# Optimization experiments

Measured on AMD Instinct MI355X. Metric: run time of the kernel, lower is better.

Reference implementation:

```python
import jax, jax.numpy as jnp
import numpy as np

N_HEADS = 16
DIM = 1024
NEG_INF = -1e20  # neginf for fp32 per original module


def setup_inputs() -> dict:
    key = jax.random.key(0)
    ks = jax.random.split(key, 10)
    B, N, D = 2, 2048, DIM
    std = np.sqrt(2.0 / (D + D))  # xavier_normal for square weights
    inp = {
        "query": jax.random.normal(ks[0], (B, N, D), dtype=jnp.float32),
        "mask": jax.random.randint(ks[1], (B, N), 0, 2, dtype=jnp.int32),
        "wq": jax.random.normal(ks[2], (D, D), dtype=jnp.float32) * std,
        "bq": jnp.zeros((D,), dtype=jnp.float32),
        "wk": jax.random.normal(ks[3], (D, D), dtype=jnp.float32) * std,
        "bk": jnp.zeros((D,), dtype=jnp.float32),
        "wv": jax.random.normal(ks[4], (D, D), dtype=jnp.float32) * std,
        "bv": jnp.zeros((D,), dtype=jnp.float32),
        "wo": jax.random.normal(ks[5], (D, D), dtype=jnp.float32) * std,
        "bo": jnp.zeros((D,), dtype=jnp.float32),
    }
    return inp


def reference(query, mask, wq, bq, wk, bk, wv, bv, wo, bo):
    B, N, D = query.shape
    H = N_HEADS
    dh = D // H
    scale = jnp.asarray(np.sqrt(dh), dtype=query.dtype)

    def heads(x):  # [B,N,D] -> [B,H,N,dh]
        return x.reshape(B, N, H, dh).transpose(0, 2, 1, 3)

    q = heads(query @ wq.T + bq) / scale
    k = heads(query @ wk.T + bk)
    v = heads(query @ wv.T + bv)

    # [B,H,Nq,Nk] scaled dot-product scores, masked where mask==0
    dot_prod = jnp.einsum("bhqd,bhkd->bhqk", q, k)
    dot_prod = jnp.where(mask[:, None, None, :] == 0, NEG_INF, dot_prod)

    attn = jax.nn.softmax(dot_prod.astype(jnp.float32), axis=-1).astype(query.dtype)
    # dropout p=0 -> identity
    ctx = jnp.einsum("bhqk,bhkd->bhqd", attn, v)
    ctx = ctx.transpose(0, 2, 1, 3).reshape(B, N, D)
    out = ctx @ wo.T + bo
    # original returns dot_prod as [B*H, Nq, Nk]
    return out, dot_prod.reshape(B * H, N, N)
```

## Files before the change

### kernel.cpp

```cpp
#include <hip/hip_runtime.h>

typedef unsigned short u16;
typedef unsigned int u32;
typedef __attribute__((ext_vector_type(8))) __bf16 bf16x8;
typedef __attribute__((ext_vector_type(4))) float f32x4;

#define MFMA(a, b, c) __builtin_amdgcn_mfma_f32_16x16x32_bf16((a), (b), (c), 0, 0, 0)

__device__ __forceinline__ u16 f2bf(float f) {
  union { float f; unsigned u; } v; v.f = f;
  unsigned r = v.u + 0x7fffu + ((v.u >> 16) & 1u);
  return (u16)(r >> 16);
}

__device__ __forceinline__ void gld16(const u16* g, u16* l) {
  __builtin_amdgcn_global_load_lds(
      (const __attribute__((address_space(1))) unsigned int*)(g),
      (__attribute__((address_space(3))) unsigned int*)(l), 16, 0, 0);
}

__global__ __launch_bounds__(256) void k_cast(
    const float* __restrict__ query, const float* __restrict__ wq,
    const float* __restrict__ wk, const float* __restrict__ wv,
    const float* __restrict__ wo, u16* __restrict__ dst)
{
  size_t i = ((size_t)blockIdx.x * 256 + threadIdx.x) * 8;
  const float* src; size_t off; float sc = 1.0f;
  if (i < 4194304u)      { src = query; off = i; }
  else if (i < 5242880u) { src = wq; off = i - 4194304u; sc = 0.125f; }
  else if (i < 6291456u) { src = wk; off = i - 5242880u; }
  else if (i < 7340032u) { src = wv; off = i - 6291456u; }
  else                   { src = wo; off = i - 7340032u; }
  float4 a = *(const float4*)(src + off);
  float4 b = *(const float4*)(src + off + 4);
  alignas(16) u16 r[8] = { f2bf(a.x*sc), f2bf(a.y*sc), f2bf(a.z*sc), f2bf(a.w*sc),
                           f2bf(b.x*sc), f2bf(b.y*sc), f2bf(b.z*sc), f2bf(b.w*sc) };
  *(int4*)(dst + i) = *(int4*)r;
}

__global__ __launch_bounds__(256) void k_gemm_qkv(
    const u16* __restrict__ Ab, const u16* __restrict__ Wb,
    const float* __restrict__ bq, const float* __restrict__ bk, const float* __restrict__ bv,
    u16* __restrict__ Qh, u16* __restrict__ Kh, u16* __restrict__ Vt)
{
  const int fb = blockIdx.x;
  const int sb = (fb & 7) * 96 + (fb >> 3);
  const int n0 = (sb % 24) * 128;
  const int m0 = (sb / 24) * 128;
  const int tid = threadIdx.x;
  const int w = tid >> 6, lane = tid & 63, g = lane >> 4, l15 = lane & 15;
  const int wm = w >> 1, wn = w & 1;
  __shared__ alignas(16) u16 As[128 * 32];
  __shared__ alignas(16) u16 Bs[128 * 32];
  f32x4 acc[4][4] = {};
  for (int k0 = 0; k0 < 1024; k0 += 32) {
    __syncthreads();
#pragma unroll
    for (int t = 0; t < 2; ++t) {
      int i = t * 256 + tid;
      int row = i >> 2, ch = i & 3, sch = ch ^ (row & 3);
      gld16(Ab + (size_t)(m0 + row) * 1024 + k0 + sch * 8, As + i * 8);
    }
#pragma unroll
    for (int t = 0; t < 2; ++t) {
      int i = t * 256 + tid;
      int row = i >> 2, ch = i & 3, sch = ch ^ (row & 3);
      gld16(Wb + (size_t)(n0 + row) * 1024 + k0 + sch * 8, Bs + i * 8);
    }
    __syncthreads();
    bf16x8 af[4], bfr[4];
#pragma unroll
    for (int i = 0; i < 4; ++i) {
      int row = wm * 64 + i * 16 + l15;
      af[i] = *(const bf16x8*)(As + (row * 4 + (g ^ (row & 3))) * 8);
    }
#pragma unroll
    for (int j = 0; j < 4; ++j) {
      int row = wn * 64 + j * 16 + l15;
      bfr[j] = *(const bf16x8*)(Bs + (row * 4 + (g ^ (row & 3))) * 8);
    }
#pragma unroll
    for (int i = 0; i < 4; ++i)
#pragma unroll
      for (int j = 0; j < 4; ++j)
        acc[i][j] = MFMA(af[i], bfr[j], acc[i][j]);
  }
  const int proj = n0 >> 10;
  const float* bias = (proj == 0) ? bq : (proj == 1) ? bk : bv;
  const float bsc = (proj == 0) ? 0.125f : 1.0f;
#pragma unroll
  for (int i = 0; i < 4; ++i)
#pragma unroll
    for (int j = 0; j < 4; ++j)
#pragma unroll
      for (int jj = 0; jj < 4; ++jj) {
        int mr = m0 + wm * 64 + i * 16 + g * 4 + jj;
        int c  = n0 + wn * 64 + j * 16 + l15;
        int d = c & 1023, h = d >> 6, d64 = d & 63;
        int b = mr >> 11, n = mr & 2047;
        int bh = (b << 4) | h;
        float v = acc[i][j][jj] + bias[d] * bsc;
        if (proj == 2) {
          Vt[((size_t)bh * 64 + d64) * 2048 + n] = f2bf(v);
        } else {
          u16* dst = (proj == 0) ? Qh : Kh;
          dst[((size_t)bh * 2048 + n) * 64 + d64] = f2bf(v);
        }
      }
}

__global__ __launch_bounds__(256) void k_gemm_out(
    const u16* __restrict__ Ab, const u16* __restrict__ Wb,
    const float* __restrict__ bo, float* __restrict__ out)
{
  const int fb = blockIdx.x;
  const int sb = (fb & 7) * 32 + (fb >> 3);
  const int n0 = (sb & 7) * 128;
  const int m0 = (sb >> 3) * 128;
  const int tid = threadIdx.x;
  const int w = tid >> 6, lane = tid & 63, g = lane >> 4, l15 = lane & 15;
  const int wm = w >> 1, wn = w & 1;
  __shared__ alignas(16) u16 As[128 * 32];
  __shared__ alignas(16) u16 Bs[128 * 32];
  f32x4 acc[4][4] = {};
  for (int k0 = 0; k0 < 1024; k0 += 32) {
    __syncthreads();
#pragma unroll
    for (int t = 0; t < 2; ++t) {
      int i = t * 256 + tid;
      int row = i >> 2, ch = i & 3, sch = ch ^ (row & 3);
      gld16(Ab + (size_t)(m0 + row) * 1024 + k0 + sch * 8, As + i * 8);
    }
#pragma unroll
    for (int t = 0; t < 2; ++t) {
      int i = t * 256 + tid;
      int row = i >> 2, ch = i & 3, sch = ch ^ (row & 3);
      gld16(Wb + (size_t)(n0 + row) * 1024 + k0 + sch * 8, Bs + i * 8);
    }
    __syncthreads();
    bf16x8 af[4], bfr[4];
#pragma unroll
    for (int i = 0; i < 4; ++i) {
      int row = wm * 64 + i * 16 + l15;
      af[i] = *(const bf16x8*)(As + (row * 4 + (g ^ (row & 3))) * 8);
    }
#pragma unroll
    for (int j = 0; j < 4; ++j) {
      int row = wn * 64 + j * 16 + l15;
      bfr[j] = *(const bf16x8*)(Bs + (row * 4 + (g ^ (row & 3))) * 8);
    }
#pragma unroll
    for (int i = 0; i < 4; ++i)
#pragma unroll
      for (int j = 0; j < 4; ++j)
        acc[i][j] = MFMA(af[i], bfr[j], acc[i][j]);
  }
#pragma unroll
  for (int i = 0; i < 4; ++i)
#pragma unroll
    for (int j = 0; j < 4; ++j)
#pragma unroll
      for (int jj = 0; jj < 4; ++jj) {
        int mr = m0 + wm * 64 + i * 16 + g * 4 + jj;
        int c  = n0 + wn * 64 + j * 16 + l15;
        out[(size_t)mr * 1024 + c] = acc[i][j][jj] + bo[c];
      }
}

__global__ __launch_bounds__(256) void k_attn(
    const u16* __restrict__ Qh, const u16* __restrict__ Kh, const u16* __restrict__ Vt,
    const int* __restrict__ mask, float* __restrict__ dout, u16* __restrict__ ctx)
{
  const int fb = blockIdx.x;
  const int sb = (fb & 7) * 128 + (fb >> 3);
  const int qt = sb & 31;
  const int bh = sb >> 5;
  const int b  = bh >> 4;
  const int tid = threadIdx.x;
  const int w = tid >> 6, lane = tid & 63, g = lane >> 4, l15 = lane & 15;
  __shared__ alignas(16) u16 Ks[128 * 64];
  __shared__ alignas(16) u16 Vs[64 * 128];
  __shared__ alignas(16) u16 Ps[4][16 * 140];

  const u16* Qrow = Qh + ((size_t)bh * 2048 + qt * 64 + w * 16 + l15) * 64;
  bf16x8 qf0 = *(const bf16x8*)(Qrow + g * 8);
  bf16x8 qf1 = *(const bf16x8*)(Qrow + 32 + g * 8);

  float m[4] = {-3e38f, -3e38f, -3e38f, -3e38f};
  float l[4] = {0.f, 0.f, 0.f, 0.f};
  f32x4 O[4] = {};
  const int* maskb = mask + b * 2048;
  float* Sbase = dout + 4194304 + (size_t)bh * 4194304
               + (size_t)(qt * 64 + w * 16 + g * 4) * 2048 + l15;

  for (int kt = 0; kt < 16; ++kt) {
    __syncthreads();
    const u16* Kg = Kh + ((size_t)bh * 2048 + kt * 128) * 64;
#pragma unroll
    for (int it = 0; it < 4; ++it) {
      int i = it * 256 + tid;
      int row = i >> 3, ch = i & 7, sch = ch ^ (row & 7);
      gld16(Kg + row * 64 + sch * 8, Ks + i * 8);
    }
    const u16* Vg = Vt + (size_t)bh * 131072 + kt * 128;
#pragma unroll
    for (int it = 0; it < 4; ++it) {
      int i = it * 256 + tid;
      int row = i >> 4, ch = i & 15, sch = ch ^ (row & 15);
      gld16(Vg + (size_t)row * 2048 + sch * 8, Vs + i * 8);
    }
    int mk[8];
#pragma unroll
    for (int f = 0; f < 8; ++f) mk[f] = maskb[kt * 128 + f * 16 + l15];
    __syncthreads();

    f32x4 s[8];
#pragma unroll
    for (int f = 0; f < 8; ++f) {
      int row = f * 16 + l15;
      bf16x8 kf0 = *(const bf16x8*)(Ks + (row * 8 + ((0 + g) ^ (row & 7))) * 8);
      bf16x8 kf1 = *(const bf16x8*)(Ks + (row * 8 + ((4 + g) ^ (row & 7))) * 8);
      f32x4 t = {};
      t = MFMA(qf0, kf0, t);
      t = MFMA(qf1, kf1, t);
      s[f] = t;
    }

    float fb8[8];
#pragma unroll
    for (int f = 0; f < 8; ++f) fb8[f] = (mk[f] != 0) ? 0.f : -1e20f;

    float mloc[4] = {-3e38f, -3e38f, -3e38f, -3e38f};
#pragma unroll
    for (int jj = 0; jj < 4; ++jj)
#pragma unroll
      for (int f = 0; f < 8; ++f) {
        float sv = s[f][jj] + fb8[f];
        s[f][jj] = sv;
        __builtin_nontemporal_store(sv, &Sbase[(size_t)jj * 2048 + kt * 128 + f * 16]);
        mloc[jj] = fmaxf(mloc[jj], sv);
      }
#pragma unroll
    for (int d = 1; d < 16; d <<= 1)
#pragma unroll
      for (int jj = 0; jj < 4; ++jj)
        mloc[jj] = fmaxf(mloc[jj], __shfl_xor(mloc[jj], d, 64));

    float corr[4];
#pragma unroll
    for (int jj = 0; jj < 4; ++jj) {
      float mn = fmaxf(m[jj], mloc[jj]);
      corr[jj] = __expf(m[jj] - mn);
      m[jj] = mn;
    }
    float psum[4] = {0.f, 0.f, 0.f, 0.f};
#pragma unroll
    for (int f = 0; f < 8; ++f)
#pragma unroll
      for (int jj = 0; jj < 4; ++jj) {
        float p = __expf(s[f][jj] - m[jj]);
        psum[jj] += p;
        Ps[w][(g * 4 + jj) * 140 + f * 16 + l15] = f2bf(p);
      }
#pragma unroll
    for (int d = 1; d < 16; d <<= 1)
#pragma unroll
      for (int jj = 0; jj < 4; ++jj)
        psum[jj] += __shfl_xor(psum[jj], d, 64);
#pragma unroll
    for (int jj = 0; jj < 4; ++jj) l[jj] = l[jj] * corr[jj] + psum[jj];
#pragma unroll
    for (int fd = 0; fd < 4; ++fd)
#pragma unroll
      for (int jj = 0; jj < 4; ++jj) O[fd][jj] *= corr[jj];

#pragma unroll
    for (int fk = 0; fk < 4; ++fk) {
      bf16x8 pa = *(const bf16x8*)(&Ps[w][l15 * 140 + fk * 32 + g * 8]);
#pragma unroll
      for (int fd = 0; fd < 4; ++fd) {
        int row = fd * 16 + l15;
        bf16x8 bv = *(const bf16x8*)(Vs + (row * 16 + ((fk * 4 + g) ^ (row & 15))) * 8);
        O[fd] = MFMA(pa, bv, O[fd]);
      }
    }
  }
  float inv[4];
#pragma unroll
  for (int jj = 0; jj < 4; ++jj) inv[jj] = 1.0f / l[jj];
  const int h = bh & 15;
#pragma unroll
  for (int fd = 0; fd < 4; ++fd)
#pragma unroll
    for (int jj = 0; jj < 4; ++jj) {
      int n = qt * 64 + w * 16 + g * 4 + jj;
      int c = h * 64 + fd * 16 + l15;
      ctx[((size_t)(b * 2048 + n)) * 1024 + c] = f2bf(O[fd][jj] * inv[jj]);
    }
}

extern "C" void kernel_launch(void* const* d_in, const int* in_sizes, int n_in,
                              void* d_out, int out_size, void* d_ws, size_t ws_size,
                              hipStream_t stream)
{
  const float* query = (const float*)d_in[0];
  const int*   mask  = (const int*)d_in[1];
  const float* wq = (const float*)d_in[2];
  const float* bq = (const float*)d_in[3];
  const float* wk = (const float*)d_in[4];
  const float* bk = (const float*)d_in[5];
  const float* wv = (const float*)d_in[6];
  const float* bv = (const float*)d_in[7];
  const float* wo = (const float*)d_in[8];
  const float* bo = (const float*)d_in[9];
  float* out = (float*)d_out;

  u16* ws   = (u16*)d_ws;
  u16* Ab   = ws;
  u16* Wqkv = ws + 4194304;
  u16* Wo   = ws + 7340032;
  u16* Qh   = ws + 8388608;
  u16* Kh   = ws + 12582912;
  u16* Vt   = ws + 16777216;
  u16* ctx  = ws + 20971520;

  k_cast<<<4096, 256, 0, stream>>>(query, wq, wk, wv, wo, ws);
  k_gemm_qkv<<<768, 256, 0, stream>>>(Ab, Wqkv, bq, bk, bv, Qh, Kh, Vt);
  k_attn<<<1024, 256, 0, stream>>>(Qh, Kh, Vt, mask, out, ctx);
  k_gemm_out<<<256, 256, 0, stream>>>(ctx, Wo, bo, out);
}
```

Baseline: 210.2 us.

## Process two 64-row query groups per attention block to reuse K/V tiles

```diff
diff --git a/kernel.cpp b/kernel.cpp
--- a/kernel.cpp
+++ b/kernel.cpp
@@ -172,9 +172,9 @@
     const int* __restrict__ mask, float* __restrict__ dout, u16* __restrict__ ctx)
 {
   const int fb = blockIdx.x;
-  const int sb = (fb & 7) * 128 + (fb >> 3);
-  const int qt = sb & 31;
-  const int bh = sb >> 5;
+  const int sb = (fb & 7) * 64 + (fb >> 3);
+  const int qt = sb & 15;
+  const int bh = sb >> 4;
   const int b  = bh >> 4;
   const int tid = threadIdx.x;
   const int w = tid >> 6, lane = tid & 63, g = lane >> 4, l15 = lane & 15;
@@ -182,16 +182,24 @@
   __shared__ alignas(16) u16 Vs[64 * 128];
   __shared__ alignas(16) u16 Ps[4][16 * 140];
 
-  const u16* Qrow = Qh + ((size_t)bh * 2048 + qt * 64 + w * 16 + l15) * 64;
-  bf16x8 qf0 = *(const bf16x8*)(Qrow + g * 8);
-  bf16x8 qf1 = *(const bf16x8*)(Qrow + 32 + g * 8);
-
-  float m[4] = {-3e38f, -3e38f, -3e38f, -3e38f};
-  float l[4] = {0.f, 0.f, 0.f, 0.f};
-  f32x4 O[4] = {};
+  bf16x8 qf0[2], qf1[2];
+#pragma unroll
+  for (int grp = 0; grp < 2; ++grp) {
+    const u16* Qrow = Qh + ((size_t)bh * 2048 + qt * 128 + grp * 64 + w * 16 + l15) * 64;
+    qf0[grp] = *(const bf16x8*)(Qrow + g * 8);
+    qf1[grp] = *(const bf16x8*)(Qrow + 32 + g * 8);
+  }
+
+  float m[2][4], l[2][4];
+  f32x4 O[2][4] = {};
+#pragma unroll
+  for (int grp = 0; grp < 2; ++grp)
+#pragma unroll
+    for (int jj = 0; jj < 4; ++jj) { m[grp][jj] = -3e38f; l[grp][jj] = 0.f; }
+
   const int* maskb = mask + b * 2048;
-  float* Sbase = dout + 4194304 + (size_t)bh * 4194304
-               + (size_t)(qt * 64 + w * 16 + g * 4) * 2048 + l15;
+  float* Sb0 = dout + 4194304 + (size_t)bh * 4194304
+             + (size_t)(qt * 128 + w * 16 + g * 4) * 2048 + l15;
 
   for (int kt = 0; kt < 16; ++kt) {
     __syncthreads();
@@ -212,91 +220,97 @@
     int mk[8];
 #pragma unroll
     for (int f = 0; f < 8; ++f) mk[f] = maskb[kt * 128 + f * 16 + l15];
-    __syncthreads();
-
-    f32x4 s[8];
-#pragma unroll
-    for (int f = 0; f < 8; ++f) {
-      int row = f * 16 + l15;
-      bf16x8 kf0 = *(const bf16x8*)(Ks + (row * 8 + ((0 + g) ^ (row & 7))) * 8);
-      bf16x8 kf1 = *(const bf16x8*)(Ks + (row * 8 + ((4 + g) ^ (row & 7))) * 8);
-      f32x4 t = {};
-      t = MFMA(qf0, kf0, t);
-      t = MFMA(qf1, kf1, t);
-      s[f] = t;
-    }
-
     float fb8[8];
 #pragma unroll
     for (int f = 0; f < 8; ++f) fb8[f] = (mk[f] != 0) ? 0.f : -1e20f;
-
-    float mloc[4] = {-3e38f, -3e38f, -3e38f, -3e38f};
-#pragma unroll
-    for (int jj = 0; jj < 4; ++jj)
+    __syncthreads();
+
+#pragma unroll
+    for (int grp = 0; grp < 2; ++grp) {
+      f32x4 s[8];
 #pragma unroll
       for (int f = 0; f < 8; ++f) {
-        float sv = s[f][jj] + fb8[f];
-        s[f][jj] = sv;
-        __builtin_nontemporal_store(sv, &Sbase[(size_t)jj * 2048 + kt * 128 + f * 16]);
-        mloc[jj] = fmaxf(mloc[jj], sv);
-      }
-#pragma unroll
-    for (int d = 1; d < 16; d <<= 1)
+        int row = f * 16 + l15;
+        bf16x8 kf0 = *(const bf16x8*)(Ks + (row * 8 + ((0 + g) ^ (row & 7))) * 8);
+        bf16x8 kf1 = *(const bf16x8*)(Ks + (row * 8 + ((4 + g) ^ (row & 7))) * 8);
+        f32x4 t = {};
+        t = MFMA(qf0[grp], kf0, t);
+        t = MFMA(qf1[grp], kf1, t);
+        s[f] = t;
+      }
+
+      float* Sbase = Sb0 + (size_t)grp * 64 * 2048;
+      float mloc[4] = {-3e38f, -3e38f, -3e38f, -3e38f};
 #pragma unroll
       for (int jj = 0; jj < 4; ++jj)
-        mloc[jj] = fmaxf(mloc[jj], __shfl_xor(mloc[jj], d, 64));
-
-    float corr[4];
-#pragma unroll
-    for (int jj = 0; jj < 4; ++jj) {
-      float mn = fmaxf(m[jj], mloc[jj]);
-      corr[jj] = __expf(m[jj] - mn);
-      m[jj] = mn;
-    }
-    float psum[4] = {0.f, 0.f, 0.f, 0.f};
-#pragma unroll
-    for (int f = 0; f < 8; ++f)
+#pragma unroll
+        for (int f = 0; f < 8; ++f) {
+          float sv = s[f][jj] + fb8[f];
+          s[f][jj] = sv;
+          __builtin_nontemporal_store(sv, &Sbase[(size_t)jj * 2048 + kt * 128 + f * 16]);
+          mloc[jj] = fmaxf(mloc[jj], sv);
+        }
+#pragma unroll
+      for (int d = 1; d < 16; d <<= 1)
+#pragma unroll
+        for (int jj = 0; jj < 4; ++jj)
+          mloc[jj] = fmaxf(mloc[jj], __shfl_xor(mloc[jj], d, 64));
+
+      float corr[4];
 #pragma unroll
       for (int jj = 0; jj < 4; ++jj) {
-        float p = __expf(s[f][jj] - m[jj]);
-        psum[jj] += p;
-        Ps[w][(g * 4 + jj) * 140 + f * 16 + l15] = f2bf(p);
-      }
-#pragma unroll
-    for (int d = 1; d < 16; d <<= 1)
-#pragma unroll
-      for (int jj = 0; jj < 4; ++jj)
-        psum[jj] += __shfl_xor(psum[jj], d, 64);
-#pragma unroll
-    for (int jj = 0; jj < 4; ++jj) l[jj] = l[jj] * corr[jj] + psum[jj];
+        float mn = fmaxf(m[grp][jj], mloc[jj]);
+        corr[jj] = __expf(m[grp][jj] - mn);
+        m[grp][jj] = mn;
+      }
+      float psum[4] = {0.f, 0.f, 0.f, 0.f};
+#pragma unroll
+      for (int f = 0; f < 8; ++f)
+#pragma unroll
+        for (int jj = 0; jj < 4; ++jj) {
+          float p = __expf(s[f][jj] - m[grp][jj]);
+          psum[jj] += p;
+          Ps[w][(g * 4 + jj) * 140 + f * 16 + l15] = f2bf(p);
+        }
+#pragma unroll
+      for (int d = 1; d < 16; d <<= 1)
+#pragma unroll
+        for (int jj = 0; jj < 4; ++jj)
+          psum[jj] += __shfl_xor(psum[jj], d, 64);
+#pragma unroll
+      for (int jj = 0; jj < 4; ++jj) l[grp][jj] = l[grp][jj] * corr[jj] + psum[jj];
+#pragma unroll
+      for (int fd = 0; fd < 4; ++fd)
+#pragma unroll
+        for (int jj = 0; jj < 4; ++jj) O[grp][fd][jj] *= corr[jj];
+
+#pragma unroll
+      for (int fk = 0; fk < 4; ++fk) {
+        bf16x8 pa = *(const bf16x8*)(&Ps[w][l15 * 140 + fk * 32 + g * 8]);
+#pragma unroll
+        for (int fd = 0; fd < 4; ++fd) {
+          int row = fd * 16 + l15;
+          bf16x8 bv = *(const bf16x8*)(Vs + (row * 16 + ((fk * 4 + g) ^ (row & 15))) * 8);
+          O[grp][fd] = MFMA(pa, bv, O[grp][fd]);
+        }
+      }
+    }
+  }
+  const int h = bh & 15;
+#pragma unroll
+  for (int grp = 0; grp < 2; ++grp) {
+    float inv[4];
+#pragma unroll
+    for (int jj = 0; jj < 4; ++jj) inv[jj] = 1.0f / l[grp][jj];
 #pragma unroll
     for (int fd = 0; fd < 4; ++fd)
 #pragma unroll
-      for (int jj = 0; jj < 4; ++jj) O[fd][jj] *= corr[jj];
-
-#pragma unroll
-    for (int fk = 0; fk < 4; ++fk) {
-      bf16x8 pa = *(const bf16x8*)(&Ps[w][l15 * 140 + fk * 32 + g * 8]);
-#pragma unroll
-      for (int fd = 0; fd < 4; ++fd) {
-        int row = fd * 16 + l15;
-        bf16x8 bv = *(const bf16x8*)(Vs + (row * 16 + ((fk * 4 + g) ^ (row & 15))) * 8);
-        O[fd] = MFMA(pa, bv, O[fd]);
-      }
-    }
-  }
-  float inv[4];
-#pragma unroll
-  for (int jj = 0; jj < 4; ++jj) inv[jj] = 1.0f / l[jj];
-  const int h = bh & 15;
-#pragma unroll
-  for (int fd = 0; fd < 4; ++fd)
-#pragma unroll
-    for (int jj = 0; jj < 4; ++jj) {
-      int n = qt * 64 + w * 16 + g * 4 + jj;
-      int c = h * 64 + fd * 16 + l15;
-      ctx[((size_t)(b * 2048 + n)) * 1024 + c] = f2bf(O[fd][jj] * inv[jj]);
-    }
+      for (int jj = 0; jj < 4; ++jj) {
+        int n = qt * 128 + grp * 64 + w * 16 + g * 4 + jj;
+        int c = h * 64 + fd * 16 + l15;
+        ctx[((size_t)(b * 2048 + n)) * 1024 + c] = f2bf(O[grp][fd][jj] * inv[jj]);
+      }
+  }
 }
 
 extern "C" void kernel_launch(void* const* d_in, const int* in_sizes, int n_in,
@@ -326,6 +340,6 @@
 
   k_cast<<<4096, 256, 0, stream>>>(query, wq, wk, wv, wo, ws);
   k_gemm_qkv<<<768, 256, 0, stream>>>(Ab, Wqkv, bq, bk, bv, Qh, Kh, Vt);
-  k_attn<<<1024, 256, 0, stream>>>(Qh, Kh, Vt, mask, out, ctx);
+  k_attn<<<512, 256, 0, stream>>>(Qh, Kh, Vt, mask, out, ctx);
   k_gemm_out<<<256, 256, 0, stream>>>(ctx, Wo, bo, out);
 }
```

Measured after the change: 211.7 us. No clear change (+0.7%).

## Double-buffer QKV GEMM with 256x256 tiles and interleaved prefetch

Applied to the files above, without the earlier changes.

```diff
diff --git a/kernel.cpp b/kernel.cpp
--- a/kernel.cpp
+++ b/kernel.cpp
@@ -38,68 +38,136 @@
   *(int4*)(dst + i) = *(int4*)r;
 }
 
-__global__ __launch_bounds__(256) void k_gemm_qkv(
+__global__ __launch_bounds__(512, 2) void k_gemm_qkv(
     const u16* __restrict__ Ab, const u16* __restrict__ Wb,
     const float* __restrict__ bq, const float* __restrict__ bk, const float* __restrict__ bv,
     u16* __restrict__ Qh, u16* __restrict__ Kh, u16* __restrict__ Vt)
 {
   const int fb = blockIdx.x;
-  const int sb = (fb & 7) * 96 + (fb >> 3);
-  const int n0 = (sb % 24) * 128;
-  const int m0 = (sb / 24) * 128;
+  const int sb = (fb & 7) * 24 + (fb >> 3);
+  const int n0 = (sb % 12) * 256;
+  const int m0 = (sb / 12) * 256;
   const int tid = threadIdx.x;
-  const int w = tid >> 6, lane = tid & 63, g = lane >> 4, l15 = lane & 15;
-  const int wm = w >> 1, wn = w & 1;
-  __shared__ alignas(16) u16 As[128 * 32];
-  __shared__ alignas(16) u16 Bs[128 * 32];
-  f32x4 acc[4][4] = {};
-  for (int k0 = 0; k0 < 1024; k0 += 32) {
-    __syncthreads();
+  const int wid = tid >> 6, lane = tid & 63, g = lane >> 4, l15 = lane & 15;
+  const int wm = wid >> 2, wn = wid & 3;
+  __shared__ alignas(16) u16 As[2][256 * 64];
+  __shared__ alignas(16) u16 Bs[2][256 * 64];
+
+  auto stageA = [&](int buf, int half, int k0) {
 #pragma unroll
     for (int t = 0; t < 2; ++t) {
-      int i = t * 256 + tid;
-      int row = i >> 2, ch = i & 3, sch = ch ^ (row & 3);
-      gld16(Ab + (size_t)(m0 + row) * 1024 + k0 + sch * 8, As + i * 8);
-    }
+      int i = t * 512 + tid;
+      int row = i >> 3, ch = i & 7;
+      gld16(Ab + (size_t)(m0 + half * 128 + row) * 1024 + k0 + ((ch ^ (row & 7)) * 8),
+            &As[buf][(half * 128 + row) * 64 + ch * 8]);
+    }
+  };
+  auto stageB = [&](int buf, int half, int k0) {
 #pragma unroll
     for (int t = 0; t < 2; ++t) {
-      int i = t * 256 + tid;
-      int row = i >> 2, ch = i & 3, sch = ch ^ (row & 3);
-      gld16(Wb + (size_t)(n0 + row) * 1024 + k0 + sch * 8, Bs + i * 8);
-    }
-    __syncthreads();
-    bf16x8 af[4], bfr[4];
-#pragma unroll
-    for (int i = 0; i < 4; ++i) {
-      int row = wm * 64 + i * 16 + l15;
-      af[i] = *(const bf16x8*)(As + (row * 4 + (g ^ (row & 3))) * 8);
-    }
-#pragma unroll
-    for (int j = 0; j < 4; ++j) {
-      int row = wn * 64 + j * 16 + l15;
-      bfr[j] = *(const bf16x8*)(Bs + (row * 4 + (g ^ (row & 3))) * 8);
-    }
-#pragma unroll
-    for (int i = 0; i < 4; ++i)
-#pragma unroll
-      for (int j = 0; j < 4; ++j)
-        acc[i][j] = MFMA(af[i], bfr[j], acc[i][j]);
+      int i = t * 512 + tid;
+      int row = i >> 3, ch = i & 7;
+      gld16(Wb + (size_t)(n0 + half * 128 + row) * 1024 + k0 + ((ch ^ (row & 7)) * 8),
+            &Bs[buf][(half * 128 + row) * 64 + ch * 8]);
+    }
+  };
+
+  f32x4 acc[8][4] = {};
+  stageA(0, 0, 0); stageA(0, 1, 0); stageB(0, 0, 0); stageB(0, 1, 0);
+  __syncthreads();
+
+  int cur = 0;
+  for (int ks = 0; ks < 16; ++ks) {
+    const int nxt = cur ^ 1;
+    const bool pf = (ks < 15);
+    const int kn = (ks + 1) * 64;
+
+    bf16x8 af[4], bf2[4];
+    if (pf) stageA(nxt, 0, kn);
+#pragma unroll
+    for (int fr = 0; fr < 4; ++fr) {
+      int row = wm * 128 + fr * 16 + l15;
+      af[fr] = *(const bf16x8*)(&As[cur][row * 64 + ((0 * 4 + g) ^ (row & 7)) * 8]);
+    }
+#pragma unroll
+    for (int fn = 0; fn < 4; ++fn) {
+      int row = wn * 64 + fn * 16 + l15;
+      bf2[fn] = *(const bf16x8*)(&Bs[cur][row * 64 + ((0 * 4 + g) ^ (row & 7)) * 8]);
+    }
+    __builtin_amdgcn_s_setprio(1);
+#pragma unroll
+    for (int fr = 0; fr < 4; ++fr)
+#pragma unroll
+      for (int fn = 0; fn < 4; ++fn)
+        acc[fr][fn] = MFMA(af[fr], bf2[fn], acc[fr][fn]);
+    __builtin_amdgcn_s_setprio(0);
+
+    if (pf) stageA(nxt, 1, kn);
+#pragma unroll
+    for (int fr = 0; fr < 4; ++fr) {
+      int row = wm * 128 + (4 + fr) * 16 + l15;
+      af[fr] = *(const bf16x8*)(&As[cur][row * 64 + ((0 * 4 + g) ^ (row & 7)) * 8]);
+    }
+    __builtin_amdgcn_s_setprio(1);
+#pragma unroll
+    for (int fr = 0; fr < 4; ++fr)
+#pragma unroll
+      for (int fn = 0; fn < 4; ++fn)
+        acc[4 + fr][fn] = MFMA(af[fr], bf2[fn], acc[4 + fr][fn]);
+    __builtin_amdgcn_s_setprio(0);
+
+    if (pf) stageB(nxt, 0, kn);
+#pragma unroll
+    for (int fn = 0; fn < 4; ++fn) {
+      int row = wn * 64 + fn * 16 + l15;
+      bf2[fn] = *(const bf16x8*)(&Bs[cur][row * 64 + ((1 * 4 + g) ^ (row & 7)) * 8]);
+    }
+#pragma unroll
+    for (int fr = 0; fr < 4; ++fr) {
+      int row = wm * 128 + (4 + fr) * 16 + l15;
+      af[fr] = *(const bf16x8*)(&As[cur][row * 64 + ((1 * 4 + g) ^ (row & 7)) * 8]);
+    }
+    __builtin_amdgcn_s_setprio(1);
+#pragma unroll
+    for (int fr = 0; fr < 4; ++fr)
+#pragma unroll
+      for (int fn = 0; fn < 4; ++fn)
+        acc[4 + fr][fn] = MFMA(af[fr], bf2[fn], acc[4 + fr][fn]);
+    __builtin_amdgcn_s_setprio(0);
+
+    if (pf) stageB(nxt, 1, kn);
+#pragma unroll
+    for (int fr = 0; fr < 4; ++fr) {
+      int row = wm * 128 + fr * 16 + l15;
+      af[fr] = *(const bf16x8*)(&As[cur][row * 64 + ((1 * 4 + g) ^ (row & 7)) * 8]);
+    }
+    __builtin_amdgcn_s_setprio(1);
+#pragma unroll
+    for (int fr = 0; fr < 4; ++fr)
+#pragma unroll
+      for (int fn = 0; fn < 4; ++fn)
+        acc[fr][fn] = MFMA(af[fr], bf2[fn], acc[fr][fn]);
+    __builtin_amdgcn_s_setprio(0);
+
+    __syncthreads();
+    cur = nxt;
   }
+
   const int proj = n0 >> 10;
   const float* bias = (proj == 0) ? bq : (proj == 1) ? bk : bv;
   const float bsc = (proj == 0) ? 0.125f : 1.0f;
 #pragma unroll
-  for (int i = 0; i < 4; ++i)
-#pragma unroll
-    for (int j = 0; j < 4; ++j)
+  for (int fr = 0; fr < 8; ++fr)
+#pragma unroll
+    for (int fn = 0; fn < 4; ++fn)
 #pragma unroll
       for (int jj = 0; jj < 4; ++jj) {
-        int mr = m0 + wm * 64 + i * 16 + g * 4 + jj;
-        int c  = n0 + wn * 64 + j * 16 + l15;
+        int mr = m0 + wm * 128 + fr * 16 + g * 4 + jj;
+        int c  = n0 + wn * 64 + fn * 16 + l15;
         int d = c & 1023, h = d >> 6, d64 = d & 63;
         int b = mr >> 11, n = mr & 2047;
         int bh = (b << 4) | h;
-        float v = acc[i][j][jj] + bias[d] * bsc;
+        float v = acc[fr][fn][jj] + bias[d] * bsc;
         if (proj == 2) {
           Vt[((size_t)bh * 64 + d64) * 2048 + n] = f2bf(v);
         } else {
@@ -325,7 +393,7 @@
   u16* ctx  = ws + 20971520;
 
   k_cast<<<4096, 256, 0, stream>>>(query, wq, wk, wv, wo, ws);
-  k_gemm_qkv<<<768, 256, 0, stream>>>(Ab, Wqkv, bq, bk, bv, Qh, Kh, Vt);
+  k_gemm_qkv<<<192, 512, 0, stream>>>(Ab, Wqkv, bq, bk, bv, Qh, Kh, Vt);
   k_attn<<<1024, 256, 0, stream>>>(Qh, Kh, Vt, mask, out, ctx);
   k_gemm_out<<<256, 256, 0, stream>>>(ctx, Wo, bo, out);
 }
```

After: 234.7 us. 11.6% more time.

## Double-buffer K tiles and interleave softmax with PV MFMAs in attention

Applied to the files above, without the earlier changes.

```diff
diff --git a/kernel.cpp b/kernel.cpp
--- a/kernel.cpp
+++ b/kernel.cpp
@@ -178,13 +178,38 @@
   const int b  = bh >> 4;
   const int tid = threadIdx.x;
   const int w = tid >> 6, lane = tid & 63, g = lane >> 4, l15 = lane & 15;
-  __shared__ alignas(16) u16 Ks[128 * 64];
+  __shared__ alignas(16) u16 Ks[2][128 * 64];
   __shared__ alignas(16) u16 Vs[64 * 128];
-  __shared__ alignas(16) u16 Ps[4][16 * 140];
+  __shared__ alignas(16) u16 Ps[4][16 * 40];
 
   const u16* Qrow = Qh + ((size_t)bh * 2048 + qt * 64 + w * 16 + l15) * 64;
   bf16x8 qf0 = *(const bf16x8*)(Qrow + g * 8);
   bf16x8 qf1 = *(const bf16x8*)(Qrow + 32 + g * 8);
+
+  const u16* Kb = Kh + (size_t)bh * 131072;
+  const u16* Vb = Vt + (size_t)bh * 131072;
+
+  auto stageK = [&](int buf, int kt) {
+#pragma unroll
+    for (int it = 0; it < 4; ++it) {
+      int i = it * 256 + tid;
+      int row = i >> 3, ch = i & 7, sch = ch ^ (row & 7);
+      gld16(Kb + (size_t)(kt * 128 + row) * 64 + sch * 8, &Ks[buf][i * 8]);
+    }
+  };
+  auto stageV = [&](int kt) {
+#pragma unroll
+    for (int it = 0; it < 4; ++it) {
+      int i = it * 256 + tid;
+      int row = i >> 4, ch = i & 15, sch = ch ^ (row & 15);
+      gld16(Vb + (size_t)row * 2048 + kt * 128 + sch * 8, &Vs[i * 8]);
+    }
+  };
+
+  stageK(0, 0);
+  asm volatile("s_waitcnt vmcnt(0)" ::: "memory");
+  __builtin_amdgcn_s_barrier();
+  __builtin_amdgcn_sched_barrier(0);
 
   float m[4] = {-3e38f, -3e38f, -3e38f, -3e38f};
   float l[4] = {0.f, 0.f, 0.f, 0.f};
@@ -194,32 +219,26 @@
                + (size_t)(qt * 64 + w * 16 + g * 4) * 2048 + l15;
 
   for (int kt = 0; kt < 16; ++kt) {
-    __syncthreads();
-    const u16* Kg = Kh + ((size_t)bh * 2048 + kt * 128) * 64;
-#pragma unroll
-    for (int it = 0; it < 4; ++it) {
-      int i = it * 256 + tid;
-      int row = i >> 3, ch = i & 7, sch = ch ^ (row & 7);
-      gld16(Kg + row * 64 + sch * 8, Ks + i * 8);
-    }
-    const u16* Vg = Vt + (size_t)bh * 131072 + kt * 128;
-#pragma unroll
-    for (int it = 0; it < 4; ++it) {
-      int i = it * 256 + tid;
-      int row = i >> 4, ch = i & 15, sch = ch ^ (row & 15);
-      gld16(Vg + (size_t)row * 2048 + sch * 8, Vs + i * 8);
-    }
+    const int cur = kt & 1;
+    asm volatile("s_waitcnt vmcnt(40)" ::: "memory");
+    __builtin_amdgcn_s_barrier();
+    __builtin_amdgcn_sched_barrier(0);
+
+    stageV(kt);
+    __builtin_amdgcn_sched_barrier(0);
+    stageK(cur ^ 1, (kt + 1) & 15);
+    __builtin_amdgcn_sched_barrier(0);
+
     int mk[8];
 #pragma unroll
     for (int f = 0; f < 8; ++f) mk[f] = maskb[kt * 128 + f * 16 + l15];
-    __syncthreads();
 
     f32x4 s[8];
 #pragma unroll
     for (int f = 0; f < 8; ++f) {
       int row = f * 16 + l15;
-      bf16x8 kf0 = *(const bf16x8*)(Ks + (row * 8 + ((0 + g) ^ (row & 7))) * 8);
-      bf16x8 kf1 = *(const bf16x8*)(Ks + (row * 8 + ((4 + g) ^ (row & 7))) * 8);
+      bf16x8 kf0 = *(const bf16x8*)(&Ks[cur][(row * 8 + ((0 + g) ^ (row & 7))) * 8]);
+      bf16x8 kf1 = *(const bf16x8*)(&Ks[cur][(row * 8 + ((4 + g) ^ (row & 7))) * 8]);
       f32x4 t = {};
       t = MFMA(qf0, kf0, t);
       t = MFMA(qf1, kf1, t);
@@ -253,15 +272,37 @@
       corr[jj] = __expf(m[jj] - mn);
       m[jj] = mn;
     }
+#pragma unroll
+    for (int fd = 0; fd < 4; ++fd)
+#pragma unroll
+      for (int jj = 0; jj < 4; ++jj) O[fd][jj] *= corr[jj];
+
+    asm volatile("s_waitcnt vmcnt(44)" ::: "memory");
+    __builtin_amdgcn_s_barrier();
+    __builtin_amdgcn_sched_barrier(0);
+
     float psum[4] = {0.f, 0.f, 0.f, 0.f};
 #pragma unroll
-    for (int f = 0; f < 8; ++f)
-#pragma unroll
-      for (int jj = 0; jj < 4; ++jj) {
-        float p = __expf(s[f][jj] - m[jj]);
-        psum[jj] += p;
-        Ps[w][(g * 4 + jj) * 140 + f * 16 + l15] = f2bf(p);
-      }
+    for (int r = 0; r < 4; ++r) {
+#pragma unroll
+      for (int f2 = 0; f2 < 2; ++f2) {
+        int f = r * 2 + f2;
+#pragma unroll
+        for (int jj = 0; jj < 4; ++jj) {
+          float p = __expf(s[f][jj] - m[jj]);
+          psum[jj] += p;
+          Ps[w][(g * 4 + jj) * 40 + f2 * 16 + l15] = f2bf(p);
+        }
+      }
+      bf16x8 pa = *(const bf16x8*)(&Ps[w][l15 * 40 + g * 8]);
+#pragma unroll
+      for (int fd = 0; fd < 4; ++fd) {
+        int row = fd * 16 + l15;
+        bf16x8 bv = *(const bf16x8*)(Vs + (row * 16 + ((r * 4 + g) ^ (row & 15))) * 8);
+        O[fd] = MFMA(pa, bv, O[fd]);
+      }
+    }
+
 #pragma unroll
     for (int d = 1; d < 16; d <<= 1)
 #pragma unroll
@@ -269,21 +310,6 @@
         psum[jj] += __shfl_xor(psum[jj], d, 64);
 #pragma unroll
     for (int jj = 0; jj < 4; ++jj) l[jj] = l[jj] * corr[jj] + psum[jj];
-#pragma unroll
-    for (int fd = 0; fd < 4; ++fd)
-#pragma unroll
-      for (int jj = 0; jj < 4; ++jj) O[fd][jj] *= corr[jj];
-
-#pragma unroll
-    for (int fk = 0; fk < 4; ++fk) {
-      bf16x8 pa = *(const bf16x8*)(&Ps[w][l15 * 140 + fk * 32 + g * 8]);
-#pragma unroll
-      for (int fd = 0; fd < 4; ++fd) {
-        int row = fd * 16 + l15;
-        bf16x8 bv = *(const bf16x8*)(Vs + (row * 16 + ((fk * 4 + g) ^ (row & 15))) * 8);
-        O[fd] = MFMA(pa, bv, O[fd]);
-      }
-    }
   }
   float inv[4];
 #pragma unroll
```

After: 200.7 us (median of 2 runs). -4.6%, faster.
